# Performance work log

Measured on AMD Instinct MI355X. Metric: run time of the kernel, lower is better.

## Reference

```python
import jax, jax.numpy as jnp
import numpy as np

N = 100000   # nodes
E = 1600000  # edges (avg degree 16)
D = 128      # input = hidden = out dim
L = 4        # num_layers
EPS = 1e-5   # LayerNorm eps


def setup_inputs() -> dict:
    key = jax.random.key(0)
    k0, k1, k2, k3, k4 = jax.random.split(key, 5)
    in_feat = jax.random.normal(k0, (N, D), dtype=jnp.float32)
    edge_index = jax.random.randint(k1, (2, E), 0, N, dtype=jnp.int32)
    s = 1.0 / np.sqrt(D)
    # GraphConv params per layer: lin_rel (weight+bias), lin_root (weight, no bias)
    W_rel = jax.random.uniform(k2, (L, D, D), jnp.float32, -s, s)
    b_rel = jax.random.uniform(k3, (L, D), jnp.float32, -s, s)
    W_root = jax.random.uniform(k4, (L, D, D), jnp.float32, -s, s)
    # single shared LayerNorm module in the torch code
    ln_gamma = jnp.ones((D,), jnp.float32)
    ln_beta = jnp.zeros((D,), jnp.float32)
    return {"in_feat": in_feat, "edge_index": edge_index, "W_rel": W_rel,
            "b_rel": b_rel, "W_root": W_root, "ln_gamma": ln_gamma, "ln_beta": ln_beta}


def _layer_norm(h, gamma, beta):
    mu = jnp.mean(h, axis=-1, keepdims=True)
    var = jnp.mean(jnp.square(h - mu), axis=-1, keepdims=True)
    return (h - mu) * jax.lax.rsqrt(var + EPS) * gamma + beta


def _graph_conv(h, W_r, b_r, W_rt, src, dst):
    # PyG GraphConv: out_i = lin_rel(sum_{j->i} x_j) + lin_root(x_i)
    agg = jax.ops.segment_sum(h[src], dst, num_segments=N)  # [N, D]
    return agg @ W_r + b_r + h @ W_rt


def reference(in_feat, edge_index, W_rel, b_rel, W_root, ln_gamma, ln_beta):
    src, dst = edge_index[0], edge_index[1]
    # input layer: conv -> ReLU -> LayerNorm -> dropout(p=0)
    h = _graph_conv(in_feat, W_rel[0], b_rel[0], W_root[0], src, dst)
    h = _layer_norm(jax.nn.relu(h), ln_gamma, ln_beta)
    # middle layers with residual
    for l in range(1, L - 1):
        nh = _graph_conv(h, W_rel[l], b_rel[l], W_root[l], src, dst)
        h = _layer_norm(jax.nn.relu(nh + h), ln_gamma, ln_beta)
    # output layer: conv only
    return _graph_conv(h, W_rel[L - 1], b_rel[L - 1], W_root[L - 1], src, dst)
```

## Files before the change

kernel.cpp:

```cpp
#include <hip/hip_runtime.h>
#include <cstddef>

#define N_NODES 100000
#define N_PAD   100032
#define N_EDGES 1600000
#define DIM 128
#define LN_EPS 1e-5f
#define ZROW   N_NODES
#define COL_CAP 3200000

#define B_SHIFT 9
#define B_SIZE  512
#define N_BKT   196
#define EPB     4096
#define NBLK    ((N_EDGES + EPB - 1) / EPB)

typedef short bf16x8 __attribute__((ext_vector_type(8)));
typedef float f32x4 __attribute__((ext_vector_type(4)));
typedef float f32x2 __attribute__((ext_vector_type(2)));

__device__ __forceinline__ float asf(uint u) {
    union { uint i; float f; } c; c.i = u; return c.f;
}
__device__ __forceinline__ float bf2f(uint u) { return asf(u << 16); }
__device__ __forceinline__ ushort f2bf(float x) {
    union { float f; uint i; } c; c.f = x;
    uint r = c.i + 0x7fffu + ((c.i >> 16) & 1u);
    return (ushort)(r >> 16);
}

__device__ __forceinline__ void accp(f32x2* acc, uint p) {
    f32x2 v;
    v.x = asf(p << 16);
    v.y = asf(p & 0xffff0000u);
    *acc += v;
}
__device__ __forceinline__ void accq(f32x2* a, uint4 p) {
    accp(&a[0], p.x); accp(&a[1], p.y); accp(&a[2], p.z); accp(&a[3], p.w);
}


__global__ __launch_bounds__(256) void bhist_kernel(const int* __restrict__ dst,
                                                    int* __restrict__ bcount) {
    __shared__ int lh[N_BKT];
    const int tid = threadIdx.x;
    if (tid < N_BKT) lh[tid] = 0;
    __syncthreads();
    const int base = blockIdx.x * EPB;
    #pragma unroll
    for (int k = 0; k < 16; ++k) {
        int t = base + tid + k * 256;
        if (t < N_EDGES) atomicAdd(&lh[dst[t] >> B_SHIFT], 1);
    }
    __syncthreads();
    if (tid < N_BKT && lh[tid]) atomicAdd(&bcount[tid], lh[tid]);
}

__global__ __launch_bounds__(256) void bscan_kernel(const int* __restrict__ bcount,
                                                    int* __restrict__ bstart,
                                                    int* __restrict__ gcur) {
    __shared__ int s[256];
    const int tid = threadIdx.x;
    int v = (tid < N_BKT) ? bcount[tid] : 0;
    s[tid] = v;
    __syncthreads();
    for (int off = 1; off < 256; off <<= 1) {
        int t = (tid >= off) ? s[tid - off] : 0;
        __syncthreads();
        s[tid] += t;
        __syncthreads();
    }
    if (tid < N_BKT) { int e = s[tid] - v; bstart[tid] = e; gcur[tid] = e; }
    if (tid == 0) bstart[N_BKT] = N_EDGES;
}

__global__ __launch_bounds__(256) void bscatter_kernel(const int* __restrict__ src,
                                                       const int* __restrict__ dst,
                                                       int* __restrict__ gcur,
                                                       int2* __restrict__ pairs) {
    __shared__ int lcnt[N_BKT];
    __shared__ int lbase[N_BKT];
    const int tid = threadIdx.x;
    if (tid < N_BKT) lcnt[tid] = 0;
    __syncthreads();
    const int base = blockIdx.x * EPB;
    int ls[16], ld[16];
    #pragma unroll
    for (int k = 0; k < 16; ++k) {
        int t = base + tid + k * 256;
        if (t < N_EDGES) {
            ls[k] = src[t]; ld[k] = dst[t];
            atomicAdd(&lcnt[ld[k] >> B_SHIFT], 1);
        } else ld[k] = -1;
    }
    __syncthreads();
    if (tid < N_BKT) lbase[tid] = lcnt[tid] ? atomicAdd(&gcur[tid], lcnt[tid]) : 0;
    __syncthreads();
    if (tid < N_BKT) lcnt[tid] = 0;
    __syncthreads();
    #pragma unroll
    for (int k = 0; k < 16; ++k) {
        if (ld[k] >= 0) {
            int b = ld[k] >> B_SHIFT;
            int r = atomicAdd(&lcnt[b], 1);
            pairs[lbase[b] + r] = make_int2(ls[k], ld[k]);
        }
    }
}

__global__ __launch_bounds__(256) void ndeg_kernel(const int2* __restrict__ pairs,
                                                   const int* __restrict__ bstart,
                                                   int* __restrict__ row_ptr,
                                                   int* __restrict__ bpad) {
    __shared__ int ldeg[B_SIZE];
    __shared__ int ws4[4];
    const int b = blockIdx.x;
    const int node0 = b << B_SHIFT;
    const int tid = threadIdx.x;
    ldeg[tid] = 0; ldeg[tid + 256] = 0;
    __syncthreads();
    const int beg = bstart[b], end = bstart[b + 1];
    for (int t = beg + tid; t < end; t += 256)
        atomicAdd(&ldeg[pairs[t].y - node0], 1);
    __syncthreads();
    const int d0 = (ldeg[2 * tid] + 15) & ~15;
    const int d1 = (ldeg[2 * tid + 1] + 15) & ~15;
    const int sum2 = d0 + d1;
    const int lane = tid & 63, wv = tid >> 6;
    int incl = sum2;
    #pragma unroll
    for (int off = 1; off < 64; off <<= 1) {
        int t = __shfl_up(incl, off);
        if (lane >= off) incl += t;
    }
    if (lane == 63) ws4[wv] = incl;
    __syncthreads();
    int woff = 0;
    if (wv > 0) woff += ws4[0];
    if (wv > 1) woff += ws4[1];
    if (wv > 2) woff += ws4[2];
    const int e0 = woff + incl - sum2;
    const int n0 = node0 + 2 * tid;
    if (n0 < N_NODES)     row_ptr[n0]     = e0;
    if (n0 + 1 < N_NODES) row_ptr[n0 + 1] = e0 + d0;
    if (tid == 255) bpad[b] = woff + incl;
}

__global__ __launch_bounds__(256) void pscan_kernel(const int* __restrict__ bpad,
                                                    int* __restrict__ bpadstart) {
    __shared__ int s[256];
    const int tid = threadIdx.x;
    int v = (tid < N_BKT) ? bpad[tid] : 0;
    s[tid] = v;
    __syncthreads();
    for (int off = 1; off < 256; off <<= 1) {
        int t = (tid >= off) ? s[tid - off] : 0;
        __syncthreads();
        s[tid] += t;
        __syncthreads();
    }
    if (tid < N_BKT) bpadstart[tid] = s[tid] - v;
    if (tid == N_BKT - 1) bpadstart[N_BKT] = s[tid];
}

__global__ void addbase_kernel(int* __restrict__ row_ptr, const int* __restrict__ bpadstart) {
    int n = blockIdx.x * 256 + threadIdx.x;
    if (n < N_NODES) row_ptr[n] += bpadstart[n >> B_SHIFT];
    else if (n <= N_PAD) row_ptr[n] = bpadstart[N_BKT];
}

__global__ void zfill_kernel(int4* __restrict__ col4) {
    int i = blockIdx.x * 256 + threadIdx.x;
    col4[i] = make_int4(ZROW, ZROW, ZROW, ZROW);
}

__global__ __launch_bounds__(256) void bfill_kernel(const int2* __restrict__ pairs,
                                                    const int* __restrict__ bstart,
                                                    const int* __restrict__ row_ptr,
                                                    int* __restrict__ col) {
    __shared__ int lcur[B_SIZE];
    const int b = blockIdx.x;
    const int node0 = b << B_SHIFT;
    const int tid = threadIdx.x;
    #pragma unroll
    for (int k = 0; k < 2; ++k) {
        int n = node0 + tid + k * 256;
        lcur[tid + k * 256] = (n < N_NODES) ? row_ptr[n] : 0;
    }
    __syncthreads();
    const int beg = bstart[b], end = bstart[b + 1];
    for (int t = beg + tid; t < end; t += 256) {
        int2 p = pairs[t];
        int r = atomicAdd(&lcur[p.y - node0], 1);
        col[r] = p.x;
    }
}


__global__ void cvt_kernel(const float* __restrict__ in, ushort* __restrict__ out) {
    int i = (blockIdx.x * blockDim.x + threadIdx.x) * 4;
    float4 v = *(const float4*)&in[i];
    uint2 r;
    r.x = (uint)f2bf(v.x) | ((uint)f2bf(v.y) << 16);
    r.y = (uint)f2bf(v.z) | ((uint)f2bf(v.w) << 16);
    *(uint2*)&out[i] = r;
}


__global__ void prepack_kernel(const float* __restrict__ Wrel, const float* __restrict__ Wroot,
                               ushort* __restrict__ Wp) {
    int t = blockIdx.x * blockDim.x + threadIdx.x;
    int layer = t >> 12;
    int tl = t & 4095;
    int frag = tl >> 6;
    int lane = tl & 63;
    int ks = frag >> 3, n = frag & 7;
    int c = n * 16 + (lane & 15);
    int k0 = ks * 32 + (lane >> 4) * 8;
    ushort tmp[8];
    #pragma unroll
    for (int j = 0; j < 8; ++j) {
        int kg = k0 + j;
        float w = (kg < 128) ? Wrel[layer * 16384 + kg * 128 + c]
                             : Wroot[layer * 16384 + (kg - 128) * 128 + c];
        tmp[j] = f2bf(w);
    }
    *(uint4*)&Wp[(size_t)t * 8] = *(const uint4*)tmp;
}


template <int MODE>
__global__ __launch_bounds__(256) void fused_kernel(const ushort* __restrict__ hb,
                                                    const int* __restrict__ row_ptr,
                                                    const int* __restrict__ col,
                                                    const ushort* __restrict__ Wp,
                                                    const float* __restrict__ brel,
                                                    const float* __restrict__ gamma,
                                                    const float* __restrict__ beta,
                                                    ushort* __restrict__ outb,
                                                    float* __restrict__ outf) {
    __shared__ char sX[64 * 512];
    const int tid = threadIdx.x;
    const int row0 = blockIdx.x * 64;
    const int lane = tid & 63;
    const int wv = tid >> 6;
    const int rsel = lane >> 4;
    const int c16 = lane & 15;

    for (int c = tid; c < 1024; c += 256) {
        int r = c >> 4, cb = c & 15;
        uint4 v = *(const uint4*)&hb[(size_t)(row0 + r) * 128 + cb * 8];
        *(uint4*)&sX[r * 512 + ((256 + cb * 16) ^ ((r & 7) << 4))] = v;
    }

    const uint4* h4 = (const uint4*)hb;
    for (int t = 0; t < 16; ++t) {
        const int r = wv * 16 + t;
        const int jbeg = row_ptr[row0 + r];
        const int iters = (row_ptr[row0 + r + 1] - jbeg) >> 4;
        f32x2 a[4];
        #pragma unroll
        for (int u = 0; u < 4; ++u) a[u] = (f32x2){0.f, 0.f};
        int j = jbeg + rsel;
        for (int it = 0; it < iters; ++it) {
            int s0 = col[j], s1 = col[j + 4], s2 = col[j + 8], s3 = col[j + 12];
            j += 16;
            uint4 p0 = h4[(size_t)s0 * 16 + c16];
            uint4 p1 = h4[(size_t)s1 * 16 + c16];
            uint4 p2 = h4[(size_t)s2 * 16 + c16];
            uint4 p3 = h4[(size_t)s3 * 16 + c16];
            accq(a, p0); accq(a, p1); accq(a, p2); accq(a, p3);
        }
        #pragma unroll
        for (int u = 0; u < 4; ++u) {
            float ax = a[u].x, ay = a[u].y;
            ax += __shfl_xor(ax, 16); ay += __shfl_xor(ay, 16);
            ax += __shfl_xor(ax, 32); ay += __shfl_xor(ay, 32);
            a[u].x = ax; a[u].y = ay;
        }
        if (rsel == 0) {
            uint4 o;
            o.x = (uint)f2bf(a[0].x) | ((uint)f2bf(a[0].y) << 16);
            o.y = (uint)f2bf(a[1].x) | ((uint)f2bf(a[1].y) << 16);
            o.z = (uint)f2bf(a[2].x) | ((uint)f2bf(a[2].y) << 16);
            o.w = (uint)f2bf(a[3].x) | ((uint)f2bf(a[3].y) << 16);
            *(uint4*)&sX[r * 512 + ((c16 * 16) ^ ((r & 7) << 4))] = o;
        }
    }
    __syncthreads();

    const int kg = lane >> 4;
    const int cl = lane & 15;
    const int ra = wv * 16 + cl;
    const int abase = ra * 512 + kg * 16;
    const int aswz = (ra & 7) << 4;

    f32x4 acc[8];
    #pragma unroll
    for (int n = 0; n < 8; ++n) acc[n] = (f32x4){0.f, 0.f, 0.f, 0.f};

    const uint4* bp = (const uint4*)Wp + lane;
    #pragma unroll 2
    for (int ks = 0; ks < 8; ++ks) {
        bf16x8 a = *(const bf16x8*)&sX[(abase + ks * 64) ^ aswz];
        #pragma unroll
        for (int n = 0; n < 8; ++n) {
            bf16x8 b = *(const bf16x8*)&bp[(ks * 8 + n) * 64];
            acc[n] = __builtin_amdgcn_mfma_f32_16x16x32_bf16(a, b, acc[n], 0, 0, 0);
        }
    }

    float bias[8], gg[8], bb[8];
    #pragma unroll
    for (int n = 0; n < 8; ++n) {
        int cn = n * 16 + cl;
        bias[n] = brel[cn];
        if (MODE != 2) { gg[n] = gamma[cn]; bb[n] = beta[cn]; }
    }

    #pragma unroll
    for (int reg = 0; reg < 4; ++reg) {
        const int r = wv * 16 + kg * 4 + reg;
        const size_t grow = (size_t)row0 + r;
        const bool live = grow < N_NODES;
        float v[8];
        float s = 0.f, q = 0.f;
        #pragma unroll
        for (int n = 0; n < 8; ++n) {
            float x = acc[n][reg] + bias[n];
            if (MODE == 1) {
                int cn = n * 16 + cl;
                ushort hu = *(const ushort*)&sX[r * 512 + ((256 + 2 * cn) ^ ((r & 7) << 4))];
                x += bf2f(hu);
            }
            if (MODE != 2) x = fmaxf(x, 0.f);
            v[n] = x; s += x; q += x * x;
        }
        if (MODE != 2) {
            #pragma unroll
            for (int m = 8; m >= 1; m >>= 1) { s += __shfl_xor(s, m); q += __shfl_xor(q, m); }
            float mu = s * (1.f / DIM);
            float var = q * (1.f / DIM) - mu * mu;
            float rinv = rsqrtf(var + LN_EPS);
            if (live) {
                #pragma unroll
                for (int n = 0; n < 8; ++n) {
                    float y = (v[n] - mu) * rinv * gg[n] + bb[n];
                    outb[grow * DIM + n * 16 + cl] = f2bf(y);
                }
            }
        } else {
            if (live) {
                #pragma unroll
                for (int n = 0; n < 8; ++n) outf[grow * DIM + n * 16 + cl] = v[n];
            }
        }
    }
}


static inline size_t align256(size_t x) { return (x + 255) & ~(size_t)255; }

extern "C" void kernel_launch(void* const* d_in, const int* in_sizes, int n_in,
                              void* d_out, int out_size, void* d_ws, size_t ws_size,
                              hipStream_t stream) {
    const float* in_feat = (const float*)d_in[0];
    const int*   ei      = (const int*)d_in[1];
    const float* Wrel    = (const float*)d_in[2];
    const float* brel    = (const float*)d_in[3];
    const float* Wroot   = (const float*)d_in[4];
    const float* gamma   = (const float*)d_in[5];
    const float* beta    = (const float*)d_in[6];
    float* out = (float*)d_out;

    char* ws = (char*)d_ws;
    size_t off = 0;
    int* col = (int*)(ws + off);        off = align256(off + (size_t)COL_CAP * 4);
    int2* pairs = (int2*)(ws + off);    off = align256(off + (size_t)N_EDGES * 8);
    int* row_ptr = (int*)(ws + off);    off = align256(off + (size_t)(N_PAD + 2) * 4);
    int* bcount = (int*)(ws + off);     off = align256(off + (size_t)N_BKT * 4);
    int* bstart = (int*)(ws + off);     off = align256(off + (size_t)(N_BKT + 1) * 4);
    int* gcur = (int*)(ws + off);       off = align256(off + (size_t)N_BKT * 4);
    int* bpad = (int*)(ws + off);       off = align256(off + (size_t)N_BKT * 4);
    int* bpadstart = (int*)(ws + off);  off = align256(off + (size_t)(N_BKT + 1) * 4);
    ushort* x0 = (ushort*)(ws + off);   off = align256(off + (size_t)N_PAD * DIM * 2);
    ushort* hA = (ushort*)(ws + off);   off = align256(off + (size_t)N_PAD * DIM * 2);
    ushort* hB = (ushort*)(ws + off);   off = align256(off + (size_t)N_PAD * DIM * 2);
    ushort* Wp = (ushort*)(ws + off);   off = align256(off + (size_t)4 * 256 * 128 * 2);
    (void)ws_size; (void)in_sizes; (void)n_in; (void)out_size;

    const int* src = ei;
    const int* dst = ei + N_EDGES;

    hipMemsetAsync(bcount, 0, (size_t)N_BKT * 4, stream);
    bhist_kernel<<<NBLK, 256, 0, stream>>>(dst, bcount);
    bscan_kernel<<<1, 256, 0, stream>>>(bcount, bstart, gcur);
    bscatter_kernel<<<NBLK, 256, 0, stream>>>(src, dst, gcur, pairs);
    ndeg_kernel<<<N_BKT, 256, 0, stream>>>(pairs, bstart, row_ptr, bpad);
    pscan_kernel<<<1, 256, 0, stream>>>(bpad, bpadstart);
    addbase_kernel<<<(N_PAD + 1 + 255) / 256, 256, 0, stream>>>(row_ptr, bpadstart);
    zfill_kernel<<<COL_CAP / 1024, 256, 0, stream>>>((int4*)col);
    bfill_kernel<<<N_BKT, 256, 0, stream>>>(pairs, bstart, row_ptr, col);

    const size_t padoff = (size_t)N_NODES * DIM * 2;
    const size_t padlen = (size_t)(N_PAD - N_NODES) * DIM * 2;
    hipMemsetAsync((char*)x0 + padoff, 0, padlen, stream);
    hipMemsetAsync((char*)hA + padoff, 0, padlen, stream);
    hipMemsetAsync((char*)hB + padoff, 0, padlen, stream);

    cvt_kernel<<<(N_NODES * DIM) / (4 * 256), 256, 0, stream>>>(in_feat, x0);
    prepack_kernel<<<64, 256, 0, stream>>>(Wrel, Wroot, Wp);

    const int grid = N_PAD / 64;

    fused_kernel<0><<<grid, 256, 0, stream>>>(x0, row_ptr, col, Wp, brel, gamma, beta, hA, nullptr);
    fused_kernel<1><<<grid, 256, 0, stream>>>(hA, row_ptr, col, Wp + 32768, brel + DIM, gamma, beta, hB, nullptr);
    fused_kernel<1><<<grid, 256, 0, stream>>>(hB, row_ptr, col, Wp + 2 * 32768, brel + 2 * DIM, gamma, beta, hA, nullptr);
    fused_kernel<2><<<grid, 256, 0, stream>>>(hA, row_ptr, col, Wp + 3 * 32768, brel + 3 * DIM, gamma, beta, nullptr, out);
}
```

Measured before the change: 447.7 us.

## Gather two rows per wave iteration and pad CSR tails inside bfill

Drops the separate zfill kernel that wrote the whole column buffer and instead has bfill write ZROW only into each node's padding slots after filling its edges. The aggregation loop now processes two destination rows at once per wave, issuing eight independent gathers per iteration to raise memory-level parallelism, with idle row slots reading the zero row. It also adds a min-blocks-per-CU hint of 5 to the launch bounds. The risks are extra wasted zero-row gathers when the two rows differ in degree, and higher register pressure under the tighter launch bound.

```diff
diff --git a/kernel.cpp b/kernel.cpp
--- a/kernel.cpp
+++ b/kernel.cpp
@@ -169,11 +169,6 @@
     else if (n <= N_PAD) row_ptr[n] = bpadstart[N_BKT];
 }
 
-__global__ void zfill_kernel(int4* __restrict__ col4) {
-    int i = blockIdx.x * 256 + threadIdx.x;
-    col4[i] = make_int4(ZROW, ZROW, ZROW, ZROW);
-}
-
 __global__ __launch_bounds__(256) void bfill_kernel(const int2* __restrict__ pairs,
                                                     const int* __restrict__ bstart,
                                                     const int* __restrict__ row_ptr,
@@ -193,6 +188,17 @@
         int2 p = pairs[t];
         int r = atomicAdd(&lcur[p.y - node0], 1);
         col[r] = p.x;
+    }
+    __syncthreads();
+    #pragma unroll
+    for (int k = 0; k < 2; ++k) {
+        int n = tid + k * 256;
+        int node = node0 + n;
+        if (node < N_NODES) {
+            int e = lcur[n];
+            int pe = row_ptr[node + 1];
+            for (int p = e; p < pe; ++p) col[p] = ZROW;
+        }
     }
 }
 
@@ -230,15 +236,15 @@
 
 
 template <int MODE>
-__global__ __launch_bounds__(256) void fused_kernel(const ushort* __restrict__ hb,
-                                                    const int* __restrict__ row_ptr,
-                                                    const int* __restrict__ col,
-                                                    const ushort* __restrict__ Wp,
-                                                    const float* __restrict__ brel,
-                                                    const float* __restrict__ gamma,
-                                                    const float* __restrict__ beta,
-                                                    ushort* __restrict__ outb,
-                                                    float* __restrict__ outf) {
+__global__ __launch_bounds__(256, 5) void fused_kernel(const ushort* __restrict__ hb,
+                                                       const int* __restrict__ row_ptr,
+                                                       const int* __restrict__ col,
+                                                       const ushort* __restrict__ Wp,
+                                                       const float* __restrict__ brel,
+                                                       const float* __restrict__ gamma,
+                                                       const float* __restrict__ beta,
+                                                       ushort* __restrict__ outb,
+                                                       float* __restrict__ outf) {
     __shared__ char sX[64 * 512];
     const int tid = threadIdx.x;
     const int row0 = blockIdx.x * 64;
@@ -254,29 +260,54 @@
     }
 
     const uint4* h4 = (const uint4*)hb;
-    for (int t = 0; t < 16; ++t) {
-        const int r = wv * 16 + t;
-        const int jbeg = row_ptr[row0 + r];
-        const int iters = (row_ptr[row0 + r + 1] - jbeg) >> 4;
-        f32x2 a[4];
+    #pragma unroll 1
+    for (int t = 0; t < 8; ++t) {
+        const int rA = wv * 16 + 2 * t;
+        const int rB = rA + 1;
+        const int p0 = row_ptr[row0 + rA];
+        const int p1 = row_ptr[row0 + rA + 1];
+        const int p2 = row_ptr[row0 + rA + 2];
+        const int itA = (p1 - p0) >> 4;
+        const int itB = (p2 - p1) >> 4;
+        int jA = p0 + rsel;
+        int jB = p1 + rsel;
+        const int iters = max(itA, itB);
+
+        f32x2 a[4], b[4];
         #pragma unroll
-        for (int u = 0; u < 4; ++u) a[u] = (f32x2){0.f, 0.f};
-        int j = jbeg + rsel;
+        for (int u = 0; u < 4; ++u) { a[u] = (f32x2){0.f, 0.f}; b[u] = (f32x2){0.f, 0.f}; }
+
         for (int it = 0; it < iters; ++it) {
-            int s0 = col[j], s1 = col[j + 4], s2 = col[j + 8], s3 = col[j + 12];
-            j += 16;
-            uint4 p0 = h4[(size_t)s0 * 16 + c16];
-            uint4 p1 = h4[(size_t)s1 * 16 + c16];
-            uint4 p2 = h4[(size_t)s2 * 16 + c16];
-            uint4 p3 = h4[(size_t)s3 * 16 + c16];
-            accq(a, p0); accq(a, p1); accq(a, p2); accq(a, p3);
-        }
+            int sA0 = ZROW, sA1 = ZROW, sA2 = ZROW, sA3 = ZROW;
+            int sB0 = ZROW, sB1 = ZROW, sB2 = ZROW, sB3 = ZROW;
+            if (it < itA) {
+                sA0 = col[jA]; sA1 = col[jA + 4]; sA2 = col[jA + 8]; sA3 = col[jA + 12];
+                jA += 16;
+            }
+            if (it < itB) {
+                sB0 = col[jB]; sB1 = col[jB + 4]; sB2 = col[jB + 8]; sB3 = col[jB + 12];
+                jB += 16;
+            }
+            uint4 pA0 = h4[(size_t)sA0 * 16 + c16];
+            uint4 pA1 = h4[(size_t)sA1 * 16 + c16];
+            uint4 pA2 = h4[(size_t)sA2 * 16 + c16];
+            uint4 pA3 = h4[(size_t)sA3 * 16 + c16];
+            uint4 pB0 = h4[(size_t)sB0 * 16 + c16];
+            uint4 pB1 = h4[(size_t)sB1 * 16 + c16];
+            uint4 pB2 = h4[(size_t)sB2 * 16 + c16];
+            uint4 pB3 = h4[(size_t)sB3 * 16 + c16];
+            accq(a, pA0); accq(a, pA1); accq(a, pA2); accq(a, pA3);
+            accq(b, pB0); accq(b, pB1); accq(b, pB2); accq(b, pB3);
+        }
+
         #pragma unroll
         for (int u = 0; u < 4; ++u) {
-            float ax = a[u].x, ay = a[u].y;
+            float ax = a[u].x, ay = a[u].y, bx = b[u].x, by = b[u].y;
             ax += __shfl_xor(ax, 16); ay += __shfl_xor(ay, 16);
+            bx += __shfl_xor(bx, 16); by += __shfl_xor(by, 16);
             ax += __shfl_xor(ax, 32); ay += __shfl_xor(ay, 32);
-            a[u].x = ax; a[u].y = ay;
+            bx += __shfl_xor(bx, 32); by += __shfl_xor(by, 32);
+            a[u].x = ax; a[u].y = ay; b[u].x = bx; b[u].y = by;
         }
         if (rsel == 0) {
             uint4 o;
@@ -284,7 +315,14 @@
             o.y = (uint)f2bf(a[1].x) | ((uint)f2bf(a[1].y) << 16);
             o.z = (uint)f2bf(a[2].x) | ((uint)f2bf(a[2].y) << 16);
             o.w = (uint)f2bf(a[3].x) | ((uint)f2bf(a[3].y) << 16);
-            *(uint4*)&sX[r * 512 + ((c16 * 16) ^ ((r & 7) << 4))] = o;
+            *(uint4*)&sX[rA * 512 + ((c16 * 16) ^ ((rA & 7) << 4))] = o;
+        } else if (rsel == 1) {
+            uint4 o;
+            o.x = (uint)f2bf(b[0].x) | ((uint)f2bf(b[0].y) << 16);
+            o.y = (uint)f2bf(b[1].x) | ((uint)f2bf(b[1].y) << 16);
+            o.z = (uint)f2bf(b[2].x) | ((uint)f2bf(b[2].y) << 16);
+            o.w = (uint)f2bf(b[3].x) | ((uint)f2bf(b[3].y) << 16);
+            *(uint4*)&sX[rB * 512 + ((c16 * 16) ^ ((rB & 7) << 4))] = o;
         }
     }
     __syncthreads();
@@ -399,7 +437,6 @@
     ndeg_kernel<<<N_BKT, 256, 0, stream>>>(pairs, bstart, row_ptr, bpad);
     pscan_kernel<<<1, 256, 0, stream>>>(bpad, bpadstart);
     addbase_kernel<<<(N_PAD + 1 + 255) / 256, 256, 0, stream>>>(row_ptr, bpadstart);
-    zfill_kernel<<<COL_CAP / 1024, 256, 0, stream>>>((int4*)col);
     bfill_kernel<<<N_BKT, 256, 0, stream>>>(pairs, bstart, row_ptr, col);
 
     const size_t padoff = (size_t)N_NODES * DIM * 2;
```

Result: faster. 425.4 us (-5.0%).
